# Optimization experiments

Hardware: AMD Instinct MI355X
Metric: run time of the kernel (lower is better)

The kernel has to match this reference:

```python
import jax, jax.numpy as jnp
import numpy as np

V = 128
L = 128
N = 4096

_ALPHA = "abcdefghijklmnopqrstuvwxyz"
TOKENS = (list("+-*/^()=") + [f"temp_{a}" for a in _ALPHA]
          + [str(d) for d in range(10)] + [f"w{i}" for i in range(84)])
assert len(TOKENS) == V
IDX = {t: i for i, t in enumerate(TOKENS)}
TEMPS = [f"temp_{a}" for a in _ALPHA]


def _build_mask_table() -> np.ndarray:
    """mask_table[p, v] = 0 if token v is illegal after prev-token p, else 1.
    Mirrors RuleFilter.single_filter's rho for every possible prev token."""
    M = np.ones((V, V), dtype=np.float32)

    def ban(prev_tokens, banned_tokens):
        cols = [IDX[t] for t in banned_tokens]
        for p in prev_tokens:
            M[IDX[p], cols] = 0.0

    ban(list("+-*/"), list("+-*/)="))          # prev is binary op
    ban(TEMPS, list("(="))                      # prev is temp_* variable
    ban(["="], list("+-*/=)") + TEMPS)         # prev is '='
    ban(["("], list("()+-*/="))                # prev is '('
    ban([")"], list("()") + TEMPS)             # prev is ')'
    ban(["^"], list("+-*/=)"))                 # prev is '^'
    return M


def setup_inputs() -> dict:
    key = jax.random.key(0)
    logits = jax.random.normal(key, (L, N, V), dtype=jnp.float32)
    mask_table = jnp.asarray(_build_mask_table())  # (V, V) rule lookup
    return {"logits": logits, "mask_table": mask_table}


def reference(logits, mask_table):
    """logits: (L, N, V); mask_table: (V, V). Sequential rule masking:
    logits[i] *= mask_table[argmax(filtered logits[i-1])]."""
    first = logits[0]  # row 0 is never filtered

    def step(carry, cur):
        # carry: previously *filtered* logits row (N, V)
        prev_idx = jnp.argmax(carry, axis=-1)          # (N,)
        new = cur * mask_table[prev_idx]               # gather + multiply
        return new, new

    _, rest = jax.lax.scan(step, first, logits[1:])
    return jnp.concatenate([first[None], rest], axis=0)
```

## Files before the change

### kernel.cpp

```cpp
#include <hip/hip_runtime.h>


constexpr int V = 128;
constexpr int L = 128;
constexpr int N = 4096;
constexpr int D = 16;
constexpr unsigned ROWB = (unsigned)N * V * 4;

typedef __attribute__((ext_vector_type(2))) float f32x2;

__device__ __forceinline__ float wave_max_dpp(float x) {
    int v = __float_as_int(x);
    const int ninf = __float_as_int(-__builtin_inff());
#define RF_STEP(ctrl)                                                          \
    {                                                                          \
        int s = __builtin_amdgcn_update_dpp(ninf, v, ctrl, 0xf, 0xf, false);   \
        v = __float_as_int(fmaxf(__int_as_float(v), __int_as_float(s)));       \
    }
    RF_STEP(0x111)
    RF_STEP(0x112)
    RF_STEP(0x114)
    RF_STEP(0x118)
    RF_STEP(0x142)
    RF_STEP(0x143)
#undef RF_STEP
    return __int_as_float(__builtin_amdgcn_readlane(v, 63));
}

__device__ __forceinline__ int wave_argmax(f32x2 f) {
    const float bv = wave_max_dpp(fmaxf(f.x, f.y));
    unsigned long long b0 = __ballot(f.x == bv);
    unsigned long long b1 = __ballot(f.y == bv);
    int i0 = __ffsll(b0);
    int i1 = __ffsll(b1);
    int c0 = i0 ? (i0 - 1) * 2 : (1 << 30);
    int c1 = i1 ? (i1 - 1) * 2 + 1 : (1 << 30);
    return min(c0, c1);
}

__device__ __forceinline__ unsigned sel8(const unsigned* t, int j) {
    unsigned a0 = (j & 1) ? t[1] : t[0];
    unsigned a1 = (j & 1) ? t[3] : t[2];
    unsigned a2 = (j & 1) ? t[5] : t[4];
    unsigned a3 = (j & 1) ? t[7] : t[6];
    unsigned b0 = (j & 2) ? a1 : a0;
    unsigned b1 = (j & 2) ? a3 : a2;
    return (j & 4) ? b1 : b0;
}

__device__ __forceinline__ unsigned long long uniform_u64(const void* p) {
    unsigned long long x = (unsigned long long)p;
    unsigned lo = __builtin_amdgcn_readfirstlane((unsigned)x);
    unsigned hi = __builtin_amdgcn_readfirstlane((unsigned)(x >> 32));
    return ((unsigned long long)hi << 32) | lo;
}

template <int I>
struct Step {
    static __device__ __forceinline__ void run(f32x2* ring, f32x2* fbuf,
                                               const unsigned* tbl, int& prev,
                                               unsigned long long lbase,
                                               unsigned long long obase,
                                               unsigned laneoff) {
        constexpr int NW = (I <= 15) ? (15 + I) : ((I <= L - D - 1) ? 30 : (15 + (L - 1 - I)));
        constexpr int s  = I & (D - 1);

        asm volatile("s_waitcnt vmcnt(%c2)"
                     : "+v"(ring[s])
                     : "v"(fbuf[s]), "i"(NW));

        f32x2 c = ring[s];
        f32x2 f;
        if (I == 0) {
            f = c;
        } else {
            const unsigned word  = sel8(tbl, prev >> 4);
            const unsigned fbits = (word >> ((prev & 15) * 2)) & 3u;
            f.x = (fbits & 1u) ? c.x : 0.0f;
            f.y = (fbits & 2u) ? c.y : 0.0f;
        }
        fbuf[s] = f;

        {
            unsigned voff = (unsigned)I * ROWB + laneoff;
            asm volatile("global_store_dwordx2 %0, %1, %2 nt"
                         :
                         : "v"(voff), "v"(fbuf[s]), "s"(obase));
        }

        prev = wave_argmax(f);

        if constexpr (I + D < L) {
            unsigned voff = (unsigned)(I + D) * ROWB + laneoff;
            asm volatile("global_load_dwordx2 %0, %1, %2"
                         : "=&v"(ring[s])
                         : "v"(voff), "s"(lbase));
        }

        Step<I + 1>::run(ring, fbuf, tbl, prev, lbase, obase, laneoff);
    }
};
template <>
struct Step<L> {
    static __device__ __forceinline__ void run(f32x2*, f32x2*, const unsigned*,
                                               int&, unsigned long long,
                                               unsigned long long, unsigned) {}
};

__global__ __launch_bounds__(256, 4) void rule_filter_kernel(
    const float* __restrict__ logits,
    const float* __restrict__ mask_table,
    float* __restrict__ out)
{
    const int wave = threadIdx.x >> 6;
    const int lane = threadIdx.x & 63;
    const int n    = (blockIdx.x << 2) + wave;

    const unsigned long long lbase = uniform_u64(logits + (size_t)n * V);
    const unsigned long long obase = uniform_u64(out    + (size_t)n * V);
    const unsigned laneoff = (unsigned)lane * 8;

    unsigned tbl[8];
#pragma unroll 1
    for (int j = 0; j < 8; ++j) {
        unsigned acc = 0;
#pragma unroll
        for (int r = 0; r < 16; ++r) {
            const int p = j * 16 + r;
            float2 mv = *(const float2*)(mask_table + (size_t)p * V + lane * 2);
            acc |= ((mv.x != 0.0f ? 1u : 0u) | (mv.y != 0.0f ? 2u : 0u)) << (2 * r);
        }
        tbl[j] = acc;
    }
    asm volatile("s_waitcnt vmcnt(0)" ::: "memory");

    f32x2 ring[D];
    f32x2 fbuf[D];
#pragma unroll
    for (int r = 0; r < D; ++r) { fbuf[r].x = 0.0f; fbuf[r].y = 0.0f; }

#pragma unroll
    for (int r = 0; r < D; ++r) {
        unsigned voff = (unsigned)r * ROWB + laneoff;
        asm volatile("global_load_dwordx2 %0, %1, %2"
                     : "=&v"(ring[r])
                     : "v"(voff), "s"(lbase));
    }

    int prev = 0;
    Step<0>::run(ring, fbuf, tbl, prev, lbase, obase, laneoff);
}

extern "C" void kernel_launch(void* const* d_in, const int* in_sizes, int n_in,
                              void* d_out, int out_size, void* d_ws, size_t ws_size,
                              hipStream_t stream) {
    const float* logits     = (const float*)d_in[0];
    const float* mask_table = (const float*)d_in[1];
    float* out              = (float*)d_out;

    dim3 grid(N / 4);
    dim3 block(256);
    rule_filter_kernel<<<grid, block, 0, stream>>>(logits, mask_table, out);
}
```

Before: 450.1 us.

## Pack two sequences per wave with 16-byte loads and half-wave argmax

Each wavefront now processes two independent sequences, one per 32-lane half, using dwordx4 loads and stores. The argmax reduction stops at 32 lanes and reads the two halves' maxima separately. The mask table is repacked with 4 bits per prev token per lane. The prefetch is issued before the wait, using a ring of D+1 slots, and the nt hint on stores is dropped. This halves the grid and cuts per-row instruction and reduction overhead, at the cost of more registers per thread and fewer waves per CU.

```diff
diff --git a/kernel.cpp b/kernel.cpp
--- a/kernel.cpp
+++ b/kernel.cpp
@@ -4,12 +4,13 @@
 constexpr int V = 128;
 constexpr int L = 128;
 constexpr int N = 4096;
-constexpr int D = 16;
+constexpr int D  = 16;
+constexpr int RD = D + 1;
 constexpr unsigned ROWB = (unsigned)N * V * 4;
 
-typedef __attribute__((ext_vector_type(2))) float f32x2;
+typedef __attribute__((ext_vector_type(4))) float f32x4;
 
-__device__ __forceinline__ float wave_max_dpp(float x) {
+__device__ __forceinline__ int halfmax_dpp(float x) {
     int v = __float_as_int(x);
     const int ninf = __float_as_int(-__builtin_inff());
 #define RF_STEP(ctrl)                                                          \
@@ -22,30 +23,36 @@
     RF_STEP(0x114)
     RF_STEP(0x118)
     RF_STEP(0x142)
-    RF_STEP(0x143)
 #undef RF_STEP
-    return __int_as_float(__builtin_amdgcn_readlane(v, 63));
+    return v;
 }
 
-__device__ __forceinline__ int wave_argmax(f32x2 f) {
-    const float bv = wave_max_dpp(fmaxf(f.x, f.y));
-    unsigned long long b0 = __ballot(f.x == bv);
-    unsigned long long b1 = __ballot(f.y == bv);
-    int i0 = __ffsll(b0);
-    int i1 = __ffsll(b1);
-    int c0 = i0 ? (i0 - 1) * 2 : (1 << 30);
-    int c1 = i1 ? (i1 - 1) * 2 + 1 : (1 << 30);
-    return min(c0, c1);
+__device__ __forceinline__ int argmax_half(unsigned m0, unsigned m1,
+                                           unsigned m2, unsigned m3) {
+    const int BIG = 1 << 30;
+    int c0 = m0 ? (__builtin_ctz(m0) * 4 + 0) : BIG;
+    int c1 = m1 ? (__builtin_ctz(m1) * 4 + 1) : BIG;
+    int c2 = m2 ? (__builtin_ctz(m2) * 4 + 2) : BIG;
+    int c3 = m3 ? (__builtin_ctz(m3) * 4 + 3) : BIG;
+    return min(min(c0, c1), min(c2, c3));
 }
 
-__device__ __forceinline__ unsigned sel8(const unsigned* t, int j) {
-    unsigned a0 = (j & 1) ? t[1] : t[0];
-    unsigned a1 = (j & 1) ? t[3] : t[2];
-    unsigned a2 = (j & 1) ? t[5] : t[4];
-    unsigned a3 = (j & 1) ? t[7] : t[6];
+__device__ __forceinline__ unsigned sel16(const unsigned* t, int j) {
+    unsigned a0 = (j & 1) ? t[1]  : t[0];
+    unsigned a1 = (j & 1) ? t[3]  : t[2];
+    unsigned a2 = (j & 1) ? t[5]  : t[4];
+    unsigned a3 = (j & 1) ? t[7]  : t[6];
+    unsigned a4 = (j & 1) ? t[9]  : t[8];
+    unsigned a5 = (j & 1) ? t[11] : t[10];
+    unsigned a6 = (j & 1) ? t[13] : t[12];
+    unsigned a7 = (j & 1) ? t[15] : t[14];
     unsigned b0 = (j & 2) ? a1 : a0;
     unsigned b1 = (j & 2) ? a3 : a2;
-    return (j & 4) ? b1 : b0;
+    unsigned b2 = (j & 2) ? a5 : a4;
+    unsigned b3 = (j & 2) ? a7 : a6;
+    unsigned c0 = (j & 4) ? b1 : b0;
+    unsigned c1 = (j & 4) ? b3 : b2;
+    return (j & 8) ? c1 : c0;
 }
 
 __device__ __forceinline__ unsigned long long uniform_u64(const void* p) {
@@ -57,98 +64,121 @@
 
 template <int I>
 struct Step {
-    static __device__ __forceinline__ void run(f32x2* ring, f32x2* fbuf,
-                                               const unsigned* tbl, int& prev,
+    static __device__ __forceinline__ void run(f32x4* ring, f32x4* fbuf,
+                                               const unsigned* tbl,
+                                               int& pA, int& pB, bool hi,
                                                unsigned long long lbase,
                                                unsigned long long obase,
                                                unsigned laneoff) {
-        constexpr int NW = (I <= 15) ? (15 + I) : ((I <= L - D - 1) ? 30 : (15 + (L - 1 - I)));
-        constexpr int s  = I & (D - 1);
+        constexpr int rs = I % RD;
+        constexpr int NW = (I < D) ? (D + I)
+            : (D - 1 + ((L - 1 - I) < (D - 1) ? (L - 1 - I) : (D - 1))
+                     + ((I <= L - 1 - D) ? 1 : 0));
+
+        if constexpr (I + D < L) {
+            constexpr int ps = (I + D) % RD;
+            unsigned voff = (unsigned)(I + D) * ROWB + laneoff;
+            asm volatile("global_load_dwordx4 %0, %1, %2"
+                         : "=&v"(ring[ps])
+                         : "v"(voff), "s"(lbase));
+        }
 
         asm volatile("s_waitcnt vmcnt(%c2)"
-                     : "+v"(ring[s])
-                     : "v"(fbuf[s]), "i"(NW));
+                     : "+v"(ring[rs])
+                     : "v"(fbuf[rs]), "i"(NW));
 
-        f32x2 c = ring[s];
-        f32x2 f;
-        if (I == 0) {
+        f32x4 c = ring[rs];
+        f32x4 f;
+        if constexpr (I == 0) {
             f = c;
         } else {
-            const unsigned word  = sel8(tbl, prev >> 4);
-            const unsigned fbits = (word >> ((prev & 15) * 2)) & 3u;
+            int pv = hi ? pB : pA;
+            unsigned word  = sel16(tbl, pv >> 3);
+            unsigned fbits = word >> ((pv & 7) * 4);
             f.x = (fbits & 1u) ? c.x : 0.0f;
             f.y = (fbits & 2u) ? c.y : 0.0f;
+            f.z = (fbits & 4u) ? c.z : 0.0f;
+            f.w = (fbits & 8u) ? c.w : 0.0f;
         }
-        fbuf[s] = f;
+        fbuf[rs] = f;
 
         {
             unsigned voff = (unsigned)I * ROWB + laneoff;
-            asm volatile("global_store_dwordx2 %0, %1, %2 nt"
+            asm volatile("global_store_dwordx4 %0, %1, %2"
                          :
-                         : "v"(voff), "v"(fbuf[s]), "s"(obase));
+                         : "v"(voff), "v"(fbuf[rs]), "s"(obase));
         }
 
-        prev = wave_argmax(f);
+        int mv  = halfmax_dpp(fmaxf(fmaxf(f.x, f.y), fmaxf(f.z, f.w)));
+        int bvA = __builtin_amdgcn_readlane(mv, 31);
+        int bvB = __builtin_amdgcn_readlane(mv, 63);
+        float bv = hi ? __int_as_float(bvB) : __int_as_float(bvA);
+        unsigned long long e0 = __ballot(f.x == bv);
+        unsigned long long e1 = __ballot(f.y == bv);
+        unsigned long long e2 = __ballot(f.z == bv);
+        unsigned long long e3 = __ballot(f.w == bv);
+        pA = argmax_half((unsigned)e0, (unsigned)e1, (unsigned)e2, (unsigned)e3);
+        pB = argmax_half((unsigned)(e0 >> 32), (unsigned)(e1 >> 32),
+                         (unsigned)(e2 >> 32), (unsigned)(e3 >> 32));
 
-        if constexpr (I + D < L) {
-            unsigned voff = (unsigned)(I + D) * ROWB + laneoff;
-            asm volatile("global_load_dwordx2 %0, %1, %2"
-                         : "=&v"(ring[s])
-                         : "v"(voff), "s"(lbase));
-        }
-
-        Step<I + 1>::run(ring, fbuf, tbl, prev, lbase, obase, laneoff);
+        Step<I + 1>::run(ring, fbuf, tbl, pA, pB, hi, lbase, obase, laneoff);
     }
 };
 template <>
 struct Step<L> {
-    static __device__ __forceinline__ void run(f32x2*, f32x2*, const unsigned*,
-                                               int&, unsigned long long,
+    static __device__ __forceinline__ void run(f32x4*, f32x4*, const unsigned*,
+                                               int&, int&, bool,
+                                               unsigned long long,
                                                unsigned long long, unsigned) {}
 };
 
-__global__ __launch_bounds__(256, 4) void rule_filter_kernel(
+__global__ __launch_bounds__(256, 2) void rule_filter_kernel(
     const float* __restrict__ logits,
     const float* __restrict__ mask_table,
     float* __restrict__ out)
 {
     const int wave = threadIdx.x >> 6;
     const int lane = threadIdx.x & 63;
-    const int n    = (blockIdx.x << 2) + wave;
+    const int ll   = lane & 31;
+    const bool hi  = lane >= 32;
+    const int pair = (blockIdx.x << 2) + wave;
 
-    const unsigned long long lbase = uniform_u64(logits + (size_t)n * V);
-    const unsigned long long obase = uniform_u64(out    + (size_t)n * V);
-    const unsigned laneoff = (unsigned)lane * 8;
+    const unsigned long long lbase = uniform_u64(logits + (size_t)pair * 2 * V);
+    const unsigned long long obase = uniform_u64(out    + (size_t)pair * 2 * V);
+    const unsigned laneoff = (unsigned)lane * 16;
 
-    unsigned tbl[8];
+    unsigned tbl[16];
 #pragma unroll 1
-    for (int j = 0; j < 8; ++j) {
+    for (int j = 0; j < 16; ++j) {
         unsigned acc = 0;
 #pragma unroll
-        for (int r = 0; r < 16; ++r) {
-            const int p = j * 16 + r;
-            float2 mv = *(const float2*)(mask_table + (size_t)p * V + lane * 2);
-            acc |= ((mv.x != 0.0f ? 1u : 0u) | (mv.y != 0.0f ? 2u : 0u)) << (2 * r);
+        for (int r = 0; r < 8; ++r) {
+            const int p = j * 8 + r;
+            float4 mv = *(const float4*)(mask_table + (size_t)p * V + ll * 4);
+            unsigned bits = (mv.x != 0.0f ? 1u : 0u) | (mv.y != 0.0f ? 2u : 0u)
+                          | (mv.z != 0.0f ? 4u : 0u) | (mv.w != 0.0f ? 8u : 0u);
+            acc |= bits << (4 * r);
         }
         tbl[j] = acc;
     }
     asm volatile("s_waitcnt vmcnt(0)" ::: "memory");
 
-    f32x2 ring[D];
-    f32x2 fbuf[D];
+    f32x4 ring[RD];
+    f32x4 fbuf[RD];
 #pragma unroll
-    for (int r = 0; r < D; ++r) { fbuf[r].x = 0.0f; fbuf[r].y = 0.0f; }
+    for (int r = 0; r < RD; ++r) { fbuf[r].x = 0.0f; fbuf[r].y = 0.0f;
+                                   fbuf[r].z = 0.0f; fbuf[r].w = 0.0f; }
 
 #pragma unroll
     for (int r = 0; r < D; ++r) {
         unsigned voff = (unsigned)r * ROWB + laneoff;
-        asm volatile("global_load_dwordx2 %0, %1, %2"
+        asm volatile("global_load_dwordx4 %0, %1, %2"
                      : "=&v"(ring[r])
                      : "v"(voff), "s"(lbase));
     }
 
-    int prev = 0;
-    Step<0>::run(ring, fbuf, tbl, prev, lbase, obase, laneoff);
+    int pA = 0, pB = 0;
+    Step<0>::run(ring, fbuf, tbl, pA, pB, hi, lbase, obase, laneoff);
 }
 
 extern "C" void kernel_launch(void* const* d_in, const int* in_sizes, int n_in,
@@ -158,7 +188,7 @@
     const float* mask_table = (const float*)d_in[1];
     float* out              = (float*)d_out;
 
-    dim3 grid(N / 4);
+    dim3 grid(N / 8);
     dim3 block(256);
     rule_filter_kernel<<<grid, block, 0, stream>>>(logits, mask_table, out);
 }
```

Result: slower. 605.9 us (+34.6%).

## Split each row across two waves with LDS argmax exchange per step

Applied to the files above, without the earlier changes.

Each sequence column n is now handled by a 128-thread block of two waves, one element per lane, instead of one wave holding two elements per lane. Each step does a wave-level max and ballot, then the two waves swap (max, index) pairs through double-buffered LDS behind a workgroup barrier to agree on the argmax. The load ring drops to depth 14 and the stores lose the nt hint. The goal is more waves in flight to hide the memory latency of the serial chain, paid for with a barrier and an LDS round trip on every one of the 128 steps.

```diff
diff --git a/kernel.cpp b/kernel.cpp
--- a/kernel.cpp
+++ b/kernel.cpp
@@ -4,10 +4,9 @@
 constexpr int V = 128;
 constexpr int L = 128;
 constexpr int N = 4096;
-constexpr int D = 16;
+constexpr int D  = 14;
+constexpr int RD = D + 1;
 constexpr unsigned ROWB = (unsigned)N * V * 4;
-
-typedef __attribute__((ext_vector_type(2))) float f32x2;
 
 __device__ __forceinline__ float wave_max_dpp(float x) {
     int v = __float_as_int(x);
@@ -27,27 +26,6 @@
     return __int_as_float(__builtin_amdgcn_readlane(v, 63));
 }
 
-__device__ __forceinline__ int wave_argmax(f32x2 f) {
-    const float bv = wave_max_dpp(fmaxf(f.x, f.y));
-    unsigned long long b0 = __ballot(f.x == bv);
-    unsigned long long b1 = __ballot(f.y == bv);
-    int i0 = __ffsll(b0);
-    int i1 = __ffsll(b1);
-    int c0 = i0 ? (i0 - 1) * 2 : (1 << 30);
-    int c1 = i1 ? (i1 - 1) * 2 + 1 : (1 << 30);
-    return min(c0, c1);
-}
-
-__device__ __forceinline__ unsigned sel8(const unsigned* t, int j) {
-    unsigned a0 = (j & 1) ? t[1] : t[0];
-    unsigned a1 = (j & 1) ? t[3] : t[2];
-    unsigned a2 = (j & 1) ? t[5] : t[4];
-    unsigned a3 = (j & 1) ? t[7] : t[6];
-    unsigned b0 = (j & 2) ? a1 : a0;
-    unsigned b1 = (j & 2) ? a3 : a2;
-    return (j & 4) ? b1 : b0;
-}
-
 __device__ __forceinline__ unsigned long long uniform_u64(const void* p) {
     unsigned long long x = (unsigned long long)p;
     unsigned lo = __builtin_amdgcn_readfirstlane((unsigned)x);
@@ -57,98 +35,133 @@
 
 template <int I>
 struct Step {
-    static __device__ __forceinline__ void run(f32x2* ring, f32x2* fbuf,
+    static __device__ __forceinline__ void run(float* ring, float* fbuf,
                                                const unsigned* tbl, int& prev,
+                                               int hbase,
                                                unsigned long long lbase,
                                                unsigned long long obase,
-                                               unsigned laneoff) {
-        constexpr int NW = (I <= 15) ? (15 + I) : ((I <= L - D - 1) ? 30 : (15 + (L - 1 - I)));
-        constexpr int s  = I & (D - 1);
+                                               unsigned laneoff,
+                                               unsigned xwa, unsigned xra) {
+        constexpr int NW = ((L - 1 - I) < D ? (L - 1 - I) : D) + (I < D ? I : D);
+        constexpr int rs = I % RD;
+
+        if constexpr (I + D < L) {
+            constexpr int ps = (I + D) % RD;
+            unsigned voff = (unsigned)(I + D) * ROWB + laneoff;
+            asm volatile("global_load_dword %0, %1, %2"
+                         : "=&v"(ring[ps])
+                         : "v"(voff), "s"(lbase));
+        }
 
         asm volatile("s_waitcnt vmcnt(%c2)"
-                     : "+v"(ring[s])
-                     : "v"(fbuf[s]), "i"(NW));
+                     : "+v"(ring[rs])
+                     : "v"(fbuf[rs]), "i"(NW));
 
-        f32x2 c = ring[s];
-        f32x2 f;
-        if (I == 0) {
+        float c = ring[rs];
+        float f;
+        if constexpr (I == 0) {
             f = c;
         } else {
-            const unsigned word  = sel8(tbl, prev >> 4);
-            const unsigned fbits = (word >> ((prev & 15) * 2)) & 3u;
-            f.x = (fbits & 1u) ? c.x : 0.0f;
-            f.y = (fbits & 2u) ? c.y : 0.0f;
+            unsigned t01  = (prev & 32) ? tbl[1] : tbl[0];
+            unsigned t23  = (prev & 32) ? tbl[3] : tbl[2];
+            unsigned word = (prev & 64) ? t23 : t01;
+            unsigned bit  = (word >> (prev & 31)) & 1u;
+            f = __int_as_float(__float_as_int(c) & (0u - bit));
         }
-        fbuf[s] = f;
+        fbuf[rs] = f;
 
         {
             unsigned voff = (unsigned)I * ROWB + laneoff;
-            asm volatile("global_store_dwordx2 %0, %1, %2 nt"
+            asm volatile("global_store_dword %0, %1, %2"
                          :
-                         : "v"(voff), "v"(fbuf[s]), "s"(obase));
+                         : "v"(voff), "v"(fbuf[rs]), "s"(obase));
         }
 
-        prev = wave_argmax(f);
+        if constexpr (I < L - 1) {
+            float bv = wave_max_dpp(f);
+            unsigned long long blt = __ballot(f == bv);
+            int im = hbase + (__ffsll((unsigned long long)blt) - 1);
 
-        if constexpr (I + D < L) {
-            unsigned voff = (unsigned)(I + D) * ROWB + laneoff;
-            asm volatile("global_load_dwordx2 %0, %1, %2"
-                         : "=&v"(ring[s])
-                         : "v"(voff), "s"(lbase));
+            unsigned long long pk =
+                ((unsigned long long)(unsigned)im << 32) |
+                (unsigned)__float_as_int(bv);
+            constexpr int PAR = (I & 1) * 1024;
+            asm volatile("ds_write_b64 %0, %1 offset:%c2"
+                         :: "v"(xwa), "v"(pk), "i"(PAR));
+            asm volatile("s_waitcnt lgkmcnt(0)");
+            __builtin_amdgcn_s_barrier();
+            unsigned long long got;
+            asm volatile("ds_read_b64 %0, %1 offset:%c2"
+                         : "=v"(got)
+                         : "v"(xra), "i"(PAR));
+            asm volatile("s_waitcnt lgkmcnt(0)" : "+v"(got));
+            __builtin_amdgcn_sched_barrier(0);
+
+            float bo = __int_as_float((int)(unsigned)(got & 0xFFFFFFFFull));
+            int   io = (int)(got >> 32);
+            bool take = (bo > bv) || ((bo == bv) && (io < im));
+            prev = take ? io : im;
         }
 
-        Step<I + 1>::run(ring, fbuf, tbl, prev, lbase, obase, laneoff);
+        Step<I + 1>::run(ring, fbuf, tbl, prev, hbase, lbase, obase, laneoff,
+                         xwa, xra);
     }
 };
 template <>
 struct Step<L> {
-    static __device__ __forceinline__ void run(f32x2*, f32x2*, const unsigned*,
-                                               int&, unsigned long long,
-                                               unsigned long long, unsigned) {}
+    static __device__ __forceinline__ void run(float*, float*, const unsigned*,
+                                               int&, int, unsigned long long,
+                                               unsigned long long, unsigned,
+                                               unsigned, unsigned) {}
 };
 
-__global__ __launch_bounds__(256, 4) void rule_filter_kernel(
+__global__ __launch_bounds__(128, 8) void rule_filter_kernel(
     const float* __restrict__ logits,
     const float* __restrict__ mask_table,
     float* __restrict__ out)
 {
-    const int wave = threadIdx.x >> 6;
+    __shared__ unsigned long long xch[2][2][64];
+
+    const int h    = threadIdx.x >> 6;
     const int lane = threadIdx.x & 63;
-    const int n    = (blockIdx.x << 2) + wave;
+    const int n    = blockIdx.x;
+    const int e    = h * 64 + lane;
 
     const unsigned long long lbase = uniform_u64(logits + (size_t)n * V);
     const unsigned long long obase = uniform_u64(out    + (size_t)n * V);
-    const unsigned laneoff = (unsigned)lane * 8;
+    const unsigned laneoff = (unsigned)e * 4;
 
-    unsigned tbl[8];
+    unsigned tbl[4];
 #pragma unroll 1
-    for (int j = 0; j < 8; ++j) {
+    for (int w = 0; w < 4; ++w) {
         unsigned acc = 0;
 #pragma unroll
-        for (int r = 0; r < 16; ++r) {
-            const int p = j * 16 + r;
-            float2 mv = *(const float2*)(mask_table + (size_t)p * V + lane * 2);
-            acc |= ((mv.x != 0.0f ? 1u : 0u) | (mv.y != 0.0f ? 2u : 0u)) << (2 * r);
+        for (int b = 0; b < 32; ++b) {
+            float m = mask_table[(size_t)(w * 32 + b) * V + e];
+            acc |= (m != 0.0f ? 1u : 0u) << b;
         }
-        tbl[j] = acc;
+        tbl[w] = acc;
     }
     asm volatile("s_waitcnt vmcnt(0)" ::: "memory");
 
-    f32x2 ring[D];
-    f32x2 fbuf[D];
+    float ring[RD];
+    float fbuf[RD];
 #pragma unroll
-    for (int r = 0; r < D; ++r) { fbuf[r].x = 0.0f; fbuf[r].y = 0.0f; }
+    for (int r = 0; r < RD; ++r) fbuf[r] = 0.0f;
 
 #pragma unroll
     for (int r = 0; r < D; ++r) {
         unsigned voff = (unsigned)r * ROWB + laneoff;
-        asm volatile("global_load_dwordx2 %0, %1, %2"
+        asm volatile("global_load_dword %0, %1, %2"
                      : "=&v"(ring[r])
                      : "v"(voff), "s"(lbase));
     }
 
+    const unsigned xwa = (unsigned)(unsigned long long)&xch[0][h][lane];
+    const unsigned xra = (unsigned)(unsigned long long)&xch[0][1 - h][lane];
+
     int prev = 0;
-    Step<0>::run(ring, fbuf, tbl, prev, lbase, obase, laneoff);
+    Step<0>::run(ring, fbuf, tbl, prev, h * 64, lbase, obase, laneoff, xwa, xra);
 }
 
 extern "C" void kernel_launch(void* const* d_in, const int* in_sizes, int n_in,
@@ -158,7 +171,7 @@
     const float* mask_table = (const float*)d_in[1];
     float* out              = (float*)d_out;
 
-    dim3 grid(N / 4);
-    dim3 block(256);
+    dim3 grid(N);
+    dim3 block(128);
     rule_filter_kernel<<<grid, block, 0, stream>>>(logits, mask_table, out);
 }
```

New measurement: 461.6 us. 2.6% more time.
